# Kernel optimization log

Hardware: AMD Instinct MI355X
Metric: run time of the kernel (lower is better)

Reference implementation:

```python
import jax, jax.numpy as jnp
import numpy as np

VOCAB, D, E, I, L, B, T = 32000, 1024, 8, 2048, 2, 4, 2048
LN_EPS = 1e-5


def setup_inputs() -> dict:
    key = jax.random.key(0)
    ks = jax.random.split(key, 10)
    return {
        "x": jax.random.randint(ks[0], (B, T), 0, VOCAB),
        "emb": jax.random.normal(ks[1], (VOCAB, D), jnp.float32) * 0.02,
        "ln_g": jnp.ones((L, D), jnp.float32),
        "ln_b": jnp.zeros((L, D), jnp.float32),
        "gate_w": jax.random.normal(ks[2], (L, D, E), jnp.float32) * 0.02,
        "gate_b": jnp.zeros((L, E), jnp.float32),
        "w1": jax.random.normal(ks[3], (L, E, D, I), jnp.float32) * 0.02,
        "w2": jax.random.normal(ks[4], (L, E, I, D), jnp.float32) * 0.02,
        "head_w": jax.random.normal(ks[5], (D, VOCAB), jnp.float32) * 0.02,
        "head_b": jnp.zeros((VOCAB,), jnp.float32),
    }


def _layer_norm(h, g, b):
    mu = jnp.mean(h, axis=-1, keepdims=True)
    var = jnp.mean(jnp.square(h - mu), axis=-1, keepdims=True)
    return (h - mu) * jax.lax.rsqrt(var + LN_EPS) * g + b


def reference(x, emb, ln_g, ln_b, gate_w, gate_b, w1, w2, head_w, head_b):
    h = emb[x]  # [B,T,D]
    experts_all = []
    for l in range(ln_g.shape[0]):  # small fixed layer loop
        xn = _layer_norm(h, ln_g[l], ln_b[l])
        gating_logits = xn @ gate_w[l] + gate_b[l]          # [B,T,E]
        rw = jax.nn.softmax(gating_logits, axis=-1)
        e = jnp.einsum('btc,eci->btei', xn, w1[l])           # [B,T,E,I]
        e = jax.nn.gelu(e, approximate=False)                # torch F.gelu default = erf
        eo = jnp.einsum('btei,eic->btec', e, w2[l])          # [B,T,E,D]
        agg = jnp.einsum('btec,bte->btc', eo, rw)
        h = h + agg
        experts_all.append(eo)
    logits = h @ head_w + head_b                             # [B,T,VOCAB]
    return logits, jnp.stack(experts_all)                    # [L,B,T,E,D]
```

## Files before the change

kernel.cpp:

```cpp
#include <hip/hip_runtime.h>
#include <hip/hip_bf16.h>
#include <stdint.h>

#define NTOK 8192
#define DM   1024
#define NE   8
#define DI   2048
#define NL   2
#define NV   32000

typedef __attribute__((ext_vector_type(8))) __bf16 bf16x8;
typedef __attribute__((ext_vector_type(4))) float  f32x4;
typedef unsigned short u16;

__device__ __forceinline__ u16 f2bf(float f) {
  uint32_t u = __builtin_bit_cast(uint32_t, f);
  return (u16)((u + 0x7fffu + ((u >> 16) & 1u)) >> 16);
}

__device__ __forceinline__ void gload_lds16(const u16* g, u16* l) {
  __builtin_amdgcn_global_load_lds(
      (const __attribute__((address_space(1))) void*)g,
      (__attribute__((address_space(3))) void*)l, 16, 0, 0);
}

__device__ __forceinline__ int xcd_swz(int orig, int nwg) {
  const int x = orig & 7, i = orig >> 3;
  const int q = nwg >> 3, r = nwg & 7;
  return (x < r ? x * (q + 1) : r * (q + 1) + (x - r) * q) + i;
}

template <int EPI>
__global__ __launch_bounds__(512) void k_gemm256(
    const u16* __restrict__ Abase, const u16* __restrict__ Wbase,
    void* __restrict__ Obase, const float* __restrict__ bias,
    int K, int mBlks, int nBlks,
    size_t aStride, size_t wStride, size_t oStride, int ldOut) {
  extern __shared__ u16 lds[];
  const int logical = xcd_swz(blockIdx.x, gridDim.x);
  const int perE = mBlks * nBlks;
  const int e    = logical / perE;
  const int rem  = logical - e * perE;
  const int nb   = rem / mBlks;
  const int mb   = rem - nb * mBlks;
  const int rowBase = mb << 8;
  const int colBase = nb << 8;
  const u16* A = Abase + (size_t)e * aStride;
  const u16* W = Wbase + (size_t)e * wStride;

  const int t = threadIdx.x;
  const int lane = t & 63, wave = t >> 6;
  const int wm = wave >> 2, wn = wave & 3;
  const int fr = lane & 15, kg = lane >> 4;

  char* sA = (char*)lds;
  char* sB = (char*)lds + 65536;

  const int c0 = t, c1 = t + 512;
  const u16* gA0 = A + (size_t)(rowBase + (c0 >> 2)) * K + (c0 & 3) * 8;
  const u16* gA1 = A + (size_t)(rowBase + (c1 >> 2)) * K + (c1 & 3) * 8;
  const u16* gB0 = W + (size_t)(colBase + (c0 >> 2)) * K + (c0 & 3) * 8;
  const u16* gB1 = W + (size_t)(colBase + (c1 >> 2)) * K + (c1 & 3) * 8;
  const int lo0 = c0 * 16, lo1 = c1 * 16;

  auto stageA = [&](int g) {
    char* dst = sA + (g & 3) * 16384;
    gload_lds16(gA0 + (size_t)g * 32, (u16*)(dst + lo0));
    gload_lds16(gA1 + (size_t)g * 32, (u16*)(dst + lo1));
  };
  auto stageB = [&](int g) {
    char* dst = sB + (g & 3) * 16384;
    gload_lds16(gB0 + (size_t)g * 32, (u16*)(dst + lo0));
    gload_lds16(gB1 + (size_t)g * 32, (u16*)(dst + lo1));
  };

  f32x4 acc[8][4] = {};
  const int NG = K >> 5;

  const int aOff = (wm * 128 + fr) * 64 + kg * 16;
  const int bOff = (wn * 64 + fr) * 64 + kg * 16;

  auto khalf = [&](int g, bool doStage) {
    __builtin_amdgcn_s_barrier();
    asm volatile("" ::: "memory");
    const char* aB = sA + (g & 3) * 16384 + aOff;
    const char* bB = sB + (g & 3) * 16384 + bOff;
    bf16x8 af[4], bv[4];
#pragma unroll
    for (int i = 0; i < 4; ++i) af[i] = *(const bf16x8*)(aB + i * 1024);
#pragma unroll
    for (int i = 0; i < 4; ++i) bv[i] = *(const bf16x8*)(bB + i * 1024);
    if (doStage) stageA(g + 3);
    __builtin_amdgcn_s_setprio(1);
#pragma unroll
    for (int mi = 0; mi < 4; ++mi)
#pragma unroll
      for (int ni = 0; ni < 4; ++ni)
        acc[mi][ni] = __builtin_amdgcn_mfma_f32_16x16x32_bf16(
            af[mi], bv[ni], acc[mi][ni], 0, 0, 0);
    __builtin_amdgcn_s_setprio(0);
    __builtin_amdgcn_s_barrier();
#pragma unroll
    for (int i = 0; i < 4; ++i) af[i] = *(const bf16x8*)(aB + 4096 + i * 1024);
    if (doStage) stageB(g + 3);
    __builtin_amdgcn_s_setprio(1);
#pragma unroll
    for (int mi = 0; mi < 4; ++mi)
#pragma unroll
      for (int ni = 0; ni < 4; ++ni)
        acc[4 + mi][ni] = __builtin_amdgcn_mfma_f32_16x16x32_bf16(
            af[mi], bv[ni], acc[4 + mi][ni], 0, 0, 0);
    __builtin_amdgcn_s_setprio(0);
  };

  stageA(0); stageB(0);
  stageA(1); stageB(1);
  stageA(2); stageB(2);

#pragma unroll 1
  for (int g = 0; g < NG - 3; ++g) {
    asm volatile("s_waitcnt vmcnt(8)" ::: "memory");
    khalf(g, true);
  }
  asm volatile("s_waitcnt vmcnt(8)" ::: "memory");
  khalf(NG - 3, false);
  asm volatile("s_waitcnt vmcnt(4)" ::: "memory");
  khalf(NG - 2, false);
  asm volatile("s_waitcnt vmcnt(0)" ::: "memory");
  khalf(NG - 1, false);

  const int row0 = rowBase + wm * 128 + (kg << 2);
  const int col0 = colBase + wn * 64 + fr;
#pragma unroll
  for (int mi = 0; mi < 8; ++mi)
#pragma unroll
    for (int ni = 0; ni < 4; ++ni) {
      const int col = col0 + ni * 16;
      const int row = row0 + mi * 16;
      if (EPI == 0) {
        float* O = (float*)Obase;
        const float bv2 = bias[col];
#pragma unroll
        for (int j = 0; j < 4; ++j)
          O[(size_t)(row + j) * ldOut + col] = acc[mi][ni][j] + bv2;
      } else if (EPI == 1) {
        u16* O = (u16*)Obase + (size_t)e * oStride;
#pragma unroll
        for (int j = 0; j < 4; ++j) {
          float v = acc[mi][ni][j];
          v = 0.5f * v * (1.0f + erff(v * 0.70710678118654752f));
          O[(size_t)(row + j) * ldOut + col] = f2bf(v);
        }
      } else {
        float* O = (float*)Obase + (size_t)e * oStride;
#pragma unroll
        for (int j = 0; j < 4; ++j)
          O[(size_t)(row + j) * ldOut + col] = acc[mi][ni][j];
      }
    }
}

__global__ void k_transcvt(const float* __restrict__ in, u16* __restrict__ out,
                           int R, int C) {
  const size_t bo = (size_t)blockIdx.z * R * C;
  in += bo; out += bo;
  __shared__ u16 tile[32][33];
  const int tx = threadIdx.x, ty = threadIdx.y;
  const int r0 = blockIdx.y << 5, c0 = blockIdx.x << 5;
#pragma unroll
  for (int j = 0; j < 4; ++j) {
    const int r = r0 + ty + j * 8;
    tile[ty + j * 8][tx] = f2bf(in[(size_t)r * C + c0 + tx]);
  }
  __syncthreads();
#pragma unroll
  for (int j = 0; j < 4; ++j) {
    const int c = c0 + ty + j * 8;
    out[(size_t)c * R + r0 + tx] = tile[tx][ty + j * 8];
  }
}

__global__ void k_gather(const int* __restrict__ x, const float* __restrict__ emb,
                         float* __restrict__ h) {
  const int n = blockIdx.x, t = threadIdx.x;
  const int id = x[n];
  ((float4*)(h + (size_t)n * DM))[t] = ((const float4*)(emb + (size_t)id * DM))[t];
}

__global__ void k_lngate(const float* __restrict__ h, const float* __restrict__ g,
                         const float* __restrict__ b, const float* __restrict__ gw,
                         const float* __restrict__ gb, u16* __restrict__ xnb,
                         float* __restrict__ rw) {
  const int n = blockIdx.x, t = threadIdx.x;
  const int wave = t >> 6, lane = t & 63;
  const float4 v = ((const float4*)(h + (size_t)n * DM))[t];
  float s = v.x + v.y + v.z + v.w;
  float q = v.x * v.x + v.y * v.y + v.z * v.z + v.w * v.w;
#pragma unroll
  for (int o = 32; o; o >>= 1) { s += __shfl_down(s, o, 64); q += __shfl_down(q, o, 64); }
  __shared__ float red[8];
  if (lane == 0) { red[wave] = s; red[wave + 4] = q; }
  __syncthreads();
  s = red[0] + red[1] + red[2] + red[3];
  q = red[4] + red[5] + red[6] + red[7];
  const float mu = s * (1.0f / DM);
  const float var = q * (1.0f / DM) - mu * mu;
  const float rs = rsqrtf(var + 1e-5f);
  const float4 gg = ((const float4*)g)[t];
  const float4 bb = ((const float4*)b)[t];
  float xv[4];
  xv[0] = (v.x - mu) * rs * gg.x + bb.x;
  xv[1] = (v.y - mu) * rs * gg.y + bb.y;
  xv[2] = (v.z - mu) * rs * gg.z + bb.z;
  xv[3] = (v.w - mu) * rs * gg.w + bb.w;
  ushort4 o4;
  o4.x = f2bf(xv[0]); o4.y = f2bf(xv[1]); o4.z = f2bf(xv[2]); o4.w = f2bf(xv[3]);
  ((ushort4*)(xnb + (size_t)n * DM))[t] = o4;
  float p[8];
#pragma unroll
  for (int e = 0; e < 8; ++e) p[e] = 0.0f;
  const float* gwp = gw + (size_t)t * 32;
#pragma unroll
  for (int j = 0; j < 4; ++j)
#pragma unroll
    for (int e = 0; e < 8; ++e) p[e] += xv[j] * gwp[j * 8 + e];
#pragma unroll
  for (int e = 0; e < 8; ++e)
#pragma unroll
    for (int o = 32; o; o >>= 1) p[e] += __shfl_down(p[e], o, 64);
  __shared__ float pr[4][8];
  if (lane == 0) {
#pragma unroll
    for (int e = 0; e < 8; ++e) pr[wave][e] = p[e];
  }
  __syncthreads();
  if (t == 0) {
    float lg[8], m = -1e30f;
#pragma unroll
    for (int e = 0; e < 8; ++e) {
      lg[e] = pr[0][e] + pr[1][e] + pr[2][e] + pr[3][e] + gb[e];
      m = fmaxf(m, lg[e]);
    }
    float ss = 0.0f;
#pragma unroll
    for (int e = 0; e < 8; ++e) { lg[e] = expf(lg[e] - m); ss += lg[e]; }
    const float inv = 1.0f / ss;
#pragma unroll
    for (int e = 0; e < 8; ++e) rw[(size_t)n * NE + e] = lg[e] * inv;
  }
}

__global__ void k_agg(float* __restrict__ h, u16* __restrict__ hbf,
                      const float* __restrict__ eo, const float* __restrict__ rw) {
  const int n = blockIdx.x, t = threadIdx.x;
  float w[8];
#pragma unroll
  for (int e = 0; e < 8; ++e) w[e] = rw[(size_t)n * NE + e];
  const float4* eo4 = (const float4*)(eo + (size_t)n * NE * DM);
  float4 a = ((float4*)(h + (size_t)n * DM))[t];
#pragma unroll
  for (int e = 0; e < 8; ++e) {
    const float4 x = eo4[e * (DM / 4) + t];
    a.x += w[e] * x.x; a.y += w[e] * x.y; a.z += w[e] * x.z; a.w += w[e] * x.w;
  }
  ((float4*)(h + (size_t)n * DM))[t] = a;
  ushort4 o4;
  o4.x = f2bf(a.x); o4.y = f2bf(a.y); o4.z = f2bf(a.z); o4.w = f2bf(a.w);
  ((ushort4*)(hbf + (size_t)n * DM))[t] = o4;
}

extern "C" void kernel_launch(void* const* d_in, const int* in_sizes, int n_in,
                              void* d_out, int out_size, void* d_ws, size_t ws_size,
                              hipStream_t stream) {
  const int*   x      = (const int*)d_in[0];
  const float* emb    = (const float*)d_in[1];
  const float* ln_g   = (const float*)d_in[2];
  const float* ln_b   = (const float*)d_in[3];
  const float* gate_w = (const float*)d_in[4];
  const float* gate_b = (const float*)d_in[5];
  const float* w1     = (const float*)d_in[6];
  const float* w2     = (const float*)d_in[7];
  const float* head_w = (const float*)d_in[8];
  const float* head_b = (const float*)d_in[9];

  float* logits  = (float*)d_out;
  float* experts = logits + (size_t)NTOK * NV;

  char* p = (char*)d_ws;
  auto carve = [&](size_t bytes) -> void* {
    void* r = (void*)p; p += (bytes + 255) & ~(size_t)255; return r;
  };
  float* h   = (float*)carve((size_t)NTOK * DM * 4);
  u16*   hbf = (u16*)  carve((size_t)NTOK * DM * 2);
  u16*   xnb = (u16*)  carve((size_t)NTOK * DM * 2);
  float* rw  = (float*)carve((size_t)NTOK * NE * 4);
  u16*   w1t = (u16*)  carve((size_t)NE * DM * DI * 2);
  u16*   w2t = (u16*)  carve((size_t)NE * DM * DI * 2);
  u16*   hwt = (u16*)  carve((size_t)NV * DM * 2);
  const size_t fixed = (size_t)(p - (char*)d_ws);
  const size_t eactOne = (size_t)NTOK * DI * 2;
  const bool batched = ws_size >= fixed + eactOne * NE;
  u16* eact = (u16*)carve(batched ? eactOne * NE : eactOne);

  hipFuncSetAttribute((const void*)k_gemm256<0>,
                      hipFuncAttributeMaxDynamicSharedMemorySize, 131072);
  hipFuncSetAttribute((const void*)k_gemm256<1>,
                      hipFuncAttributeMaxDynamicSharedMemorySize, 131072);
  hipFuncSetAttribute((const void*)k_gemm256<2>,
                      hipFuncAttributeMaxDynamicSharedMemorySize, 131072);

  k_gather<<<dim3(NTOK), dim3(256), 0, stream>>>(x, emb, h);

  for (int l = 0; l < NL; ++l) {
    k_lngate<<<dim3(NTOK), dim3(256), 0, stream>>>(
        h, ln_g + (size_t)l * DM, ln_b + (size_t)l * DM,
        gate_w + (size_t)l * DM * NE, gate_b + (size_t)l * NE, xnb, rw);
    k_transcvt<<<dim3(DI / 32, DM / 32, NE), dim3(32, 8), 0, stream>>>(
        w1 + (size_t)l * NE * DM * DI, w1t, DM, DI);
    k_transcvt<<<dim3(DM / 32, DI / 32, NE), dim3(32, 8), 0, stream>>>(
        w2 + (size_t)l * NE * DM * DI, w2t, DI, DM);
    float* expertsL = experts + (size_t)l * NTOK * NE * DM;
    if (batched) {
      k_gemm256<1><<<dim3(NE * (DI / 256) * (NTOK / 256)), dim3(512), 131072, stream>>>(
          xnb, w1t, eact, nullptr, DM, NTOK / 256, DI / 256,
          (size_t)0, (size_t)DM * DI, (size_t)NTOK * DI, DI);
      k_gemm256<2><<<dim3(NE * (DM / 256) * (NTOK / 256)), dim3(512), 131072, stream>>>(
          eact, w2t, expertsL, nullptr, DI, NTOK / 256, DM / 256,
          (size_t)NTOK * DI, (size_t)DM * DI, (size_t)DM, NE * DM);
    } else {
      for (int e = 0; e < NE; ++e) {
        k_gemm256<1><<<dim3((DI / 256) * (NTOK / 256)), dim3(512), 131072, stream>>>(
            xnb, w1t + (size_t)e * DM * DI, eact, nullptr, DM, NTOK / 256, DI / 256,
            (size_t)0, (size_t)0, (size_t)0, DI);
        k_gemm256<2><<<dim3((DM / 256) * (NTOK / 256)), dim3(512), 131072, stream>>>(
            eact, w2t + (size_t)e * DM * DI, expertsL + (size_t)e * DM, nullptr,
            DI, NTOK / 256, DM / 256, (size_t)0, (size_t)0, (size_t)0, NE * DM);
      }
    }
    k_agg<<<dim3(NTOK), dim3(256), 0, stream>>>(h, hbf, expertsL, rw);
  }

  k_transcvt<<<dim3(NV / 32, DM / 32, 1), dim3(32, 8), 0, stream>>>(head_w, hwt, DM, NV);
  k_gemm256<0><<<dim3((NV / 256) * (NTOK / 256)), dim3(512), 131072, stream>>>(
      hbf, hwt, logits, head_b, DM, NTOK / 256, NV / 256,
      (size_t)0, (size_t)0, (size_t)0, NV);
}
```

Measured before the change: 2.690 ms.

## Restructure GEMM to 128x256 tiles, 2 blocks/CU, swizzled LDS, triple buffering

Replaces the 256x256 512-thread GEMM with a 128x256 tile kernel of 256 threads targeting two blocks per CU, a 3-stage global->LDS pipeline with one barrier per k-step, and an XOR-swizzled LDS layout to reduce bank conflicts. Output stores and the expert-output reads in the aggregation kernel become nontemporal. This aims at higher occupancy, better load balance across CUs and fewer LDS conflicts, at the cost of lower operand reuse per tile and a shallower prefetch.

```diff
diff --git a/kernel.cpp b/kernel.cpp
--- a/kernel.cpp
+++ b/kernel.cpp
@@ -18,7 +18,7 @@
   return (u16)((u + 0x7fffu + ((u >> 16) & 1u)) >> 16);
 }
 
-__device__ __forceinline__ void gload_lds16(const u16* g, u16* l) {
+__device__ __forceinline__ void gload_lds16(const u16* g, void* l) {
   __builtin_amdgcn_global_load_lds(
       (const __attribute__((address_space(1))) void*)g,
       (__attribute__((address_space(3))) void*)l, 16, 0, 0);
@@ -31,105 +31,97 @@
 }
 
 template <int EPI>
-__global__ __launch_bounds__(512) void k_gemm256(
-    const u16* __restrict__ Abase, const u16* __restrict__ Wbase,
-    void* __restrict__ Obase, const float* __restrict__ bias,
+__global__ __launch_bounds__(256, 2) void k_gemm(
+    const u16* __restrict__ A0, const u16* __restrict__ W0,
+    void* __restrict__ O0, const float* __restrict__ bias,
     int K, int mBlks, int nBlks,
     size_t aStride, size_t wStride, size_t oStride, int ldOut) {
-  extern __shared__ u16 lds[];
+  extern __shared__ char lds[];
   const int logical = xcd_swz(blockIdx.x, gridDim.x);
   const int perE = mBlks * nBlks;
   const int e    = logical / perE;
   const int rem  = logical - e * perE;
   const int nb   = rem / mBlks;
   const int mb   = rem - nb * mBlks;
-  const int rowBase = mb << 8;
-  const int colBase = nb << 8;
-  const u16* A = Abase + (size_t)e * aStride;
-  const u16* W = Wbase + (size_t)e * wStride;
-
-  const int t = threadIdx.x;
-  const int lane = t & 63, wave = t >> 6;
-  const int wm = wave >> 2, wn = wave & 3;
+  const int rowBase = mb * 128;
+  const int colBase = nb * 256;
+  const u16* A = A0 + (size_t)e * aStride;
+  const u16* W = W0 + (size_t)e * wStride;
+
+  const int t = threadIdx.x, lane = t & 63, wn = t >> 6;
   const int fr = lane & 15, kg = lane >> 4;
 
-  char* sA = (char*)lds;
-  char* sB = (char*)lds + 65536;
-
-  const int c0 = t, c1 = t + 512;
-  const u16* gA0 = A + (size_t)(rowBase + (c0 >> 2)) * K + (c0 & 3) * 8;
-  const u16* gA1 = A + (size_t)(rowBase + (c1 >> 2)) * K + (c1 & 3) * 8;
-  const u16* gB0 = W + (size_t)(colBase + (c0 >> 2)) * K + (c0 & 3) * 8;
-  const u16* gB1 = W + (size_t)(colBase + (c1 >> 2)) * K + (c1 & 3) * 8;
-  const int lo0 = c0 * 16, lo1 = c1 * 16;
-
-  auto stageA = [&](int g) {
-    char* dst = sA + (g & 3) * 16384;
-    gload_lds16(gA0 + (size_t)g * 32, (u16*)(dst + lo0));
-    gload_lds16(gA1 + (size_t)g * 32, (u16*)(dst + lo1));
+  const u16* gA[2]; int loA[2];
+#pragma unroll
+  for (int i = 0; i < 2; ++i) {
+    const int c = t + 256 * i, row = c >> 2;
+    const int gs = (c & 3) ^ ((row >> 2) & 3);
+    gA[i] = A + (size_t)(rowBase + row) * K + gs * 8;
+    loA[i] = c * 16;
+  }
+  const u16* gB[4]; int loB[4];
+#pragma unroll
+  for (int j = 0; j < 4; ++j) {
+    const int c = t + 256 * j, row = c >> 2;
+    const int gs = (c & 3) ^ ((row >> 2) & 3);
+    gB[j] = W + (size_t)(colBase + row) * K + gs * 8;
+    loB[j] = 8192 + c * 16;
+  }
+
+  auto stage = [&](int g, int buf) {
+    char* dst = lds + buf * 24576;
+#pragma unroll
+    for (int i = 0; i < 2; ++i) gload_lds16(gA[i] + (size_t)g * 32, dst + loA[i]);
+#pragma unroll
+    for (int j = 0; j < 4; ++j) gload_lds16(gB[j] + (size_t)g * 32, dst + loB[j]);
   };
-  auto stageB = [&](int g) {
-    char* dst = sB + (g & 3) * 16384;
-    gload_lds16(gB0 + (size_t)g * 32, (u16*)(dst + lo0));
-    gload_lds16(gB1 + (size_t)g * 32, (u16*)(dst + lo1));
-  };
+
+  const int swzo = (kg ^ ((fr >> 2) & 3)) * 16;
+  const int aOff = fr * 64 + swzo;
+  const int bOff = 8192 + (wn * 64 + fr) * 64 + swzo;
 
   f32x4 acc[8][4] = {};
   const int NG = K >> 5;
 
-  const int aOff = (wm * 128 + fr) * 64 + kg * 16;
-  const int bOff = (wn * 64 + fr) * 64 + kg * 16;
-
-  auto khalf = [&](int g, bool doStage) {
-    __builtin_amdgcn_s_barrier();
-    asm volatile("" ::: "memory");
-    const char* aB = sA + (g & 3) * 16384 + aOff;
-    const char* bB = sB + (g & 3) * 16384 + bOff;
-    bf16x8 af[4], bv[4];
-#pragma unroll
-    for (int i = 0; i < 4; ++i) af[i] = *(const bf16x8*)(aB + i * 1024);
-#pragma unroll
-    for (int i = 0; i < 4; ++i) bv[i] = *(const bf16x8*)(bB + i * 1024);
-    if (doStage) stageA(g + 3);
+  auto compute = [&](int buf) {
+    const char* base = lds + buf * 24576;
+    bf16x8 af[8], bv[4];
+#pragma unroll
+    for (int mi = 0; mi < 8; ++mi) af[mi] = *(const bf16x8*)(base + aOff + mi * 1024);
+#pragma unroll
+    for (int ni = 0; ni < 4; ++ni) bv[ni] = *(const bf16x8*)(base + bOff + ni * 1024);
     __builtin_amdgcn_s_setprio(1);
 #pragma unroll
-    for (int mi = 0; mi < 4; ++mi)
+    for (int mi = 0; mi < 8; ++mi)
 #pragma unroll
       for (int ni = 0; ni < 4; ++ni)
         acc[mi][ni] = __builtin_amdgcn_mfma_f32_16x16x32_bf16(
             af[mi], bv[ni], acc[mi][ni], 0, 0, 0);
     __builtin_amdgcn_s_setprio(0);
+  };
+
+  stage(0, 0);
+  stage(1, 1);
+
+  int buf = 0;
+#pragma unroll 1
+  for (int g = 0; g < NG - 1; ++g) {
+    asm volatile("s_waitcnt vmcnt(6)" ::: "memory");
     __builtin_amdgcn_s_barrier();
-#pragma unroll
-    for (int i = 0; i < 4; ++i) af[i] = *(const bf16x8*)(aB + 4096 + i * 1024);
-    if (doStage) stageB(g + 3);
-    __builtin_amdgcn_s_setprio(1);
-#pragma unroll
-    for (int mi = 0; mi < 4; ++mi)
-#pragma unroll
-      for (int ni = 0; ni < 4; ++ni)
-        acc[4 + mi][ni] = __builtin_amdgcn_mfma_f32_16x16x32_bf16(
-            af[mi], bv[ni], acc[4 + mi][ni], 0, 0, 0);
-    __builtin_amdgcn_s_setprio(0);
-  };
-
-  stageA(0); stageB(0);
-  stageA(1); stageB(1);
-  stageA(2); stageB(2);
-
-#pragma unroll 1
-  for (int g = 0; g < NG - 3; ++g) {
-    asm volatile("s_waitcnt vmcnt(8)" ::: "memory");
-    khalf(g, true);
-  }
-  asm volatile("s_waitcnt vmcnt(8)" ::: "memory");
-  khalf(NG - 3, false);
-  asm volatile("s_waitcnt vmcnt(4)" ::: "memory");
-  khalf(NG - 2, false);
+    asm volatile("" ::: "memory");
+    if (g + 2 < NG) {
+      int b2 = buf + 2; if (b2 >= 3) b2 -= 3;
+      stage(g + 2, b2);
+    }
+    compute(buf);
+    ++buf; if (buf >= 3) buf = 0;
+  }
   asm volatile("s_waitcnt vmcnt(0)" ::: "memory");
-  khalf(NG - 1, false);
-
-  const int row0 = rowBase + wm * 128 + (kg << 2);
+  __builtin_amdgcn_s_barrier();
+  asm volatile("" ::: "memory");
+  compute(buf);
+
+  const int row0 = rowBase + (kg << 2);
   const int col0 = colBase + wn * 64 + fr;
 #pragma unroll
   for (int mi = 0; mi < 8; ++mi)
@@ -138,24 +130,26 @@
       const int col = col0 + ni * 16;
       const int row = row0 + mi * 16;
       if (EPI == 0) {
-        float* O = (float*)Obase;
+        float* O = (float*)O0;
         const float bv2 = bias[col];
 #pragma unroll
         for (int j = 0; j < 4; ++j)
-          O[(size_t)(row + j) * ldOut + col] = acc[mi][ni][j] + bv2;
+          __builtin_nontemporal_store(acc[mi][ni][j] + bv2,
+                                      &O[(size_t)(row + j) * ldOut + col]);
       } else if (EPI == 1) {
-        u16* O = (u16*)Obase + (size_t)e * oStride;
+        u16* O = (u16*)O0 + (size_t)e * oStride;
 #pragma unroll
         for (int j = 0; j < 4; ++j) {
           float v = acc[mi][ni][j];
           v = 0.5f * v * (1.0f + erff(v * 0.70710678118654752f));
-          O[(size_t)(row + j) * ldOut + col] = f2bf(v);
+          __builtin_nontemporal_store(f2bf(v), &O[(size_t)(row + j) * ldOut + col]);
         }
       } else {
-        float* O = (float*)Obase + (size_t)e * oStride;
+        float* O = (float*)O0 + (size_t)e * oStride;
 #pragma unroll
         for (int j = 0; j < 4; ++j)
-          O[(size_t)(row + j) * ldOut + col] = acc[mi][ni][j];
+          __builtin_nontemporal_store(acc[mi][ni][j],
+                                      &O[(size_t)(row + j) * ldOut + col]);
       }
     }
 }
@@ -256,14 +250,14 @@
   float w[8];
 #pragma unroll
   for (int e = 0; e < 8; ++e) w[e] = rw[(size_t)n * NE + e];
-  const float4* eo4 = (const float4*)(eo + (size_t)n * NE * DM);
-  float4 a = ((float4*)(h + (size_t)n * DM))[t];
+  const f32x4* eo4 = (const f32x4*)(eo + (size_t)n * NE * DM);
+  f32x4 a = ((f32x4*)(h + (size_t)n * DM))[t];
 #pragma unroll
   for (int e = 0; e < 8; ++e) {
-    const float4 x = eo4[e * (DM / 4) + t];
-    a.x += w[e] * x.x; a.y += w[e] * x.y; a.z += w[e] * x.z; a.w += w[e] * x.w;
-  }
-  ((float4*)(h + (size_t)n * DM))[t] = a;
+    const f32x4 xv = __builtin_nontemporal_load(&eo4[e * (DM / 4) + t]);
+    a += w[e] * xv;
+  }
+  ((f32x4*)(h + (size_t)n * DM))[t] = a;
   ushort4 o4;
   o4.x = f2bf(a.x); o4.y = f2bf(a.y); o4.z = f2bf(a.z); o4.w = f2bf(a.w);
   ((ushort4*)(hbf + (size_t)n * DM))[t] = o4;
@@ -302,12 +296,15 @@
   const bool batched = ws_size >= fixed + eactOne * NE;
   u16* eact = (u16*)carve(batched ? eactOne * NE : eactOne);
 
-  hipFuncSetAttribute((const void*)k_gemm256<0>,
-                      hipFuncAttributeMaxDynamicSharedMemorySize, 131072);
-  hipFuncSetAttribute((const void*)k_gemm256<1>,
-                      hipFuncAttributeMaxDynamicSharedMemorySize, 131072);
-  hipFuncSetAttribute((const void*)k_gemm256<2>,
-                      hipFuncAttributeMaxDynamicSharedMemorySize, 131072);
+  const int LDSB = 73728;
+  (void)hipFuncSetAttribute((const void*)k_gemm<0>,
+                            hipFuncAttributeMaxDynamicSharedMemorySize, LDSB);
+  (void)hipFuncSetAttribute((const void*)k_gemm<1>,
+                            hipFuncAttributeMaxDynamicSharedMemorySize, LDSB);
+  (void)hipFuncSetAttribute((const void*)k_gemm<2>,
+                            hipFuncAttributeMaxDynamicSharedMemorySize, LDSB);
+
+  const int MB = NTOK / 128;
 
   k_gather<<<dim3(NTOK), dim3(256), 0, stream>>>(x, emb, h);
 
@@ -321,27 +318,27 @@
         w2 + (size_t)l * NE * DM * DI, w2t, DI, DM);
     float* expertsL = experts + (size_t)l * NTOK * NE * DM;
     if (batched) {
-      k_gemm256<1><<<dim3(NE * (DI / 256) * (NTOK / 256)), dim3(512), 131072, stream>>>(
-          xnb, w1t, eact, nullptr, DM, NTOK / 256, DI / 256,
+      k_gemm<1><<<dim3(NE * MB * (DI / 256)), dim3(256), LDSB, stream>>>(
+          xnb, w1t, eact, nullptr, DM, MB, DI / 256,
           (size_t)0, (size_t)DM * DI, (size_t)NTOK * DI, DI);
-      k_gemm256<2><<<dim3(NE * (DM / 256) * (NTOK / 256)), dim3(512), 131072, stream>>>(
-          eact, w2t, expertsL, nullptr, DI, NTOK / 256, DM / 256,
+      k_gemm<2><<<dim3(NE * MB * (DM / 256)), dim3(256), LDSB, stream>>>(
+          eact, w2t, expertsL, nullptr, DI, MB, DM / 256,
           (size_t)NTOK * DI, (size_t)DM * DI, (size_t)DM, NE * DM);
     } else {
       for (int e = 0; e < NE; ++e) {
-        k_gemm256<1><<<dim3((DI / 256) * (NTOK / 256)), dim3(512), 131072, stream>>>(
-            xnb, w1t + (size_t)e * DM * DI, eact, nullptr, DM, NTOK / 256, DI / 256,
+        k_gemm<1><<<dim3(MB * (DI / 256)), dim3(256), LDSB, stream>>>(
+            xnb, w1t + (size_t)e * DM * DI, eact, nullptr, DM, MB, DI / 256,
             (size_t)0, (size_t)0, (size_t)0, DI);
-        k_gemm256<2><<<dim3((DM / 256) * (NTOK / 256)), dim3(512), 131072, stream>>>(
+        k_gemm<2><<<dim3(MB * (DM / 256)), dim3(256), LDSB, stream>>>(
             eact, w2t + (size_t)e * DM * DI, expertsL + (size_t)e * DM, nullptr,
-            DI, NTOK / 256, DM / 256, (size_t)0, (size_t)0, (size_t)0, NE * DM);
+            DI, MB, DM / 256, (size_t)0, (size_t)0, (size_t)0, NE * DM);
       }
     }
     k_agg<<<dim3(NTOK), dim3(256), 0, stream>>>(h, hbf, expertsL, rw);
   }
 
   k_transcvt<<<dim3(NV / 32, DM / 32, 1), dim3(32, 8), 0, stream>>>(head_w, hwt, DM, NV);
-  k_gemm256<0><<<dim3((NV / 256) * (NTOK / 256)), dim3(512), 131072, stream>>>(
-      hbf, hwt, logits, head_b, DM, NTOK / 256, NV / 256,
+  k_gemm<0><<<dim3(MB * (NV / 256)), dim3(256), LDSB, stream>>>(
+      hbf, hwt, logits, head_b, DM, MB, NV / 256,
       (size_t)0, (size_t)0, (size_t)0, NV);
 }
```

Result: no change. 2.675 ms (-0.5%).
